# Optimization experiments

Hardware: AMD Instinct MI355X
Metric: run time of the kernel (lower is better)

The kernel has to match this reference:

```python
import jax, jax.numpy as jnp
import numpy as np

N = 100000       # nodes
E = 3200000      # edges
DIN = 128        # input_dim
H = 64           # hidden_dim
DEMB = 32        # embedding_dim
G = 256          # num graphs


def setup_inputs() -> dict:
    key = jax.random.key(0)
    ks = jax.random.split(key, 10)
    x = jax.random.normal(ks[0], (N, DIN), dtype=jnp.float32)
    edge_index = jax.random.randint(ks[1], (2, E), 0, N, dtype=jnp.int64)
    batch = jnp.sort(jax.random.randint(ks[2], (N,), 0, G, dtype=jnp.int64))
    W1 = jax.random.normal(ks[3], (DIN, H), dtype=jnp.float32) * (1.0 / np.sqrt(DIN))
    b1 = jnp.zeros((H,), dtype=jnp.float32)
    W2 = jax.random.normal(ks[4], (H, H), dtype=jnp.float32) * (1.0 / np.sqrt(H))
    b2 = jnp.zeros((H,), dtype=jnp.float32)
    Wl = jax.random.normal(ks[5], (H, DEMB), dtype=jnp.float32) * (1.0 / np.sqrt(H))
    bl = jnp.zeros((DEMB,), dtype=jnp.float32)
    return {"x": x, "edge_index": edge_index, "batch": batch, "num_graphs": G,
            "W1": W1, "b1": b1, "W2": W2, "b2": b2, "Wl": Wl, "bl": bl}


def _gcn_conv(h, src, dst, W, b, n_nodes):
    # PyG GCNConv: add self-loops, symmetric D^{-1/2}(A+I)D^{-1/2} normalization,
    # linear transform first, then propagate.
    h = h @ W                                                  # [N, out]
    deg = jax.ops.segment_sum(jnp.ones((src.shape[0],), h.dtype), dst,
                              num_segments=n_nodes) + 1.0      # +1 self-loop
    dinv = jax.lax.rsqrt(deg)                                  # [N]
    coef = dinv[src] * dinv[dst]                               # [E]
    msgs = h[src] * coef[:, None]                              # [E, out]
    agg = jax.ops.segment_sum(msgs, dst, num_segments=n_nodes)
    agg = agg + h * (dinv * dinv)[:, None]                     # self-loop message
    return agg + b


def reference(x, edge_index, batch, num_graphs, W1, b1, W2, b2, Wl, bl):
    src, dst = edge_index[0], edge_index[1]
    n_nodes = x.shape[0]
    h = jax.nn.relu(_gcn_conv(x, src, dst, W1, b1, n_nodes))
    h = jax.nn.relu(_gcn_conv(h, src, dst, W2, b2, n_nodes))
    # global_mean_pool over batch ids
    sums = jax.ops.segment_sum(h, batch, num_segments=num_graphs)     # [G, H]
    counts = jax.ops.segment_sum(jnp.ones((n_nodes,), h.dtype), batch,
                                 num_segments=num_graphs)
    pooled = sums / jnp.maximum(counts, 1.0)[:, None]
    return pooled @ Wl + bl                                           # [G, DEMB]
```

## Files before the change

### kernel.cpp

```cpp
#include <hip/hip_runtime.h>

#define NN 100000
#define NE 3200000
#define DIN 128
#define HD 64
#define DEMB 32
#define NG 256
#define NBUCK ((NN + 255) / 256)
#define NPB 512
#define CHUNK ((NE + NPB - 1) / NPB)
#define NM (NBUCK * NPB)
#define NMB ((NM + 1023) / 1024)

typedef unsigned short u16;
typedef unsigned int u32;

__device__ __forceinline__ float bflo(u32 u) { return __uint_as_float(u << 16); }
__device__ __forceinline__ float bfhi(u32 u) { return __uint_as_float(u & 0xffff0000u); }
__device__ __forceinline__ u16 f2bf(float f) {
    u32 u = __float_as_uint(f);
    return (u16)((u + 0x7fffu + ((u >> 16) & 1u)) >> 16);
}

__global__ __launch_bounds__(256) void k_blkhist(const int* __restrict__ dst,
                                                 int* __restrict__ HM, int E) {
    __shared__ int h[NBUCK];
    int blk = blockIdx.x, t = threadIdx.x;
    for (int i = t; i < NBUCK; i += 256) h[i] = 0;
    __syncthreads();
    int beg = blk * CHUNK, end = min(E, beg + CHUNK);
    for (int j = beg + t; j < end; j += 256) atomicAdd(&h[dst[j] >> 8], 1);
    __syncthreads();
    for (int i = t; i < NBUCK; i += 256) HM[i * NPB + blk] = h[i];
}

__global__ __launch_bounds__(1024) void k_scanA(int* __restrict__ HM,
                                                int* __restrict__ bsum, int n) {
    __shared__ int s[1024];
    int t = threadIdx.x;
    int idx = blockIdx.x * 1024 + t;
    int v = (idx < n) ? HM[idx] : 0;
    s[t] = v;
    __syncthreads();
    for (int off = 1; off < 1024; off <<= 1) {
        int add = (t >= off) ? s[t - off] : 0;
        __syncthreads();
        s[t] += add;
        __syncthreads();
    }
    if (idx < n) HM[idx] = s[t] - v;
    if (t == 1023) bsum[blockIdx.x] = s[t];
}

__global__ __launch_bounds__(256) void k_scan2(const int* __restrict__ bsum,
                                               int* __restrict__ boff, int nb) {
    __shared__ int s[256];
    int t = threadIdx.x;
    int v = (t < nb) ? bsum[t] : 0;
    s[t] = v;
    __syncthreads();
    for (int off = 1; off < 256; off <<= 1) {
        int add = (t >= off) ? s[t - off] : 0;
        __syncthreads();
        s[t] += add;
        __syncthreads();
    }
    if (t < nb) boff[t] = s[t] - v;
    if (t == nb - 1) boff[nb] = s[t];
}

__global__ void k_scanC(int* __restrict__ HM, const int* __restrict__ boff, int n) {
    int idx = blockIdx.x * blockDim.x + threadIdx.x;
    if (idx < n) HM[idx] += boff[idx >> 10];
}

__global__ __launch_bounds__(256) void k_place(const int* __restrict__ src,
                                               const int* __restrict__ dst,
                                               const int* __restrict__ HM,
                                               int* __restrict__ part, int E) {
    __shared__ int cur[NBUCK];
    int blk = blockIdx.x, t = threadIdx.x;
    for (int i = t; i < NBUCK; i += 256) cur[i] = HM[i * NPB + blk];
    __syncthreads();
    int beg = blk * CHUNK, end = min(E, beg + CHUNK);
    for (int j = beg + t; j < end; j += 256) {
        int d = dst[j], s = src[j];
        int pos = atomicAdd(&cur[d >> 8], 1);
        part[pos] = s | ((d & 255) << 17);
    }
}

__global__ __launch_bounds__(256) void k_phaseB(const int* __restrict__ part,
                                                const int* __restrict__ HM,
                                                int* __restrict__ rowptr,
                                                int* __restrict__ ssrc,
                                                float* __restrict__ dinv, int E) {
    __shared__ int cnt[256];
    __shared__ int sc[256];
    int b = blockIdx.x;
    int t = threadIdx.x;
    int beg = HM[b * NPB];
    int end = (b == NBUCK - 1) ? E : HM[(b + 1) * NPB];
    int node0 = b << 8;
    int nnode = NN - node0 < 256 ? NN - node0 : 256;
    cnt[t] = 0;
    __syncthreads();
    for (int j = beg + t; j < end; j += 256) atomicAdd(&cnt[part[j] >> 17], 1);
    __syncthreads();
    int v = cnt[t];
    sc[t] = v;
    __syncthreads();
    for (int off = 1; off < 256; off <<= 1) {
        int add = (t >= off) ? sc[t - off] : 0;
        __syncthreads();
        sc[t] += add;
        __syncthreads();
    }
    int excl = sc[t] - v;
    if (t < nnode) {
        rowptr[node0 + t] = beg + excl;
        dinv[node0 + t] = rsqrtf((float)v + 1.0f);
    }
    if (b == NBUCK - 1 && t == 0) rowptr[NN] = E;
    __syncthreads();
    cnt[t] = beg + excl;
    __syncthreads();
    for (int j = beg + t; j < end; j += 256) {
        int e = part[j];
        int pos = atomicAdd(&cnt[e >> 17], 1);
        ssrc[pos] = e & 0x1FFFF;
    }
}

template <int K, typename XT>
__global__ __launch_bounds__(256, 4) void k_gemm(const XT* __restrict__ X,
                                                 const float* __restrict__ W,
                                                 const float* __restrict__ dinv,
                                                 u16* __restrict__ U, int n) {
    __shared__ __align__(16) float xt[32][68];
    __shared__ __align__(16) float wlc[32][64];
    int tid = threadIdx.x;
    int cg = tid & 15;
    int rs = tid >> 4;
    int row0 = blockIdx.x * 64;
    float4 acc0 = {0.f, 0.f, 0.f, 0.f};
    float4 acc1 = {0.f, 0.f, 0.f, 0.f};
    float4 acc2 = {0.f, 0.f, 0.f, 0.f};
    float4 acc3 = {0.f, 0.f, 0.f, 0.f};
    for (int kc = 0; kc < K; kc += 32) {
        __syncthreads();
        for (int p = 0; p < 2; ++p) {
            int idx = tid + p * 256;
            int r = idx >> 3;
            int c4 = idx & 7;
            int row = row0 + r;
            float4 v = {0.f, 0.f, 0.f, 0.f};
            if (row < n) {
                if constexpr (sizeof(XT) == 4) {
                    v = *reinterpret_cast<const float4*>(&X[(size_t)row * K + kc + c4 * 4]);
                } else {
                    ushort4 b = *reinterpret_cast<const ushort4*>(&X[(size_t)row * K + kc + c4 * 4]);
                    v.x = __uint_as_float((u32)b.x << 16);
                    v.y = __uint_as_float((u32)b.y << 16);
                    v.z = __uint_as_float((u32)b.z << 16);
                    v.w = __uint_as_float((u32)b.w << 16);
                }
            }
            xt[c4 * 4 + 0][r] = v.x;
            xt[c4 * 4 + 1][r] = v.y;
            xt[c4 * 4 + 2][r] = v.z;
            xt[c4 * 4 + 3][r] = v.w;
        }
        for (int p = 0; p < 2; ++p) {
            int idx = tid + p * 256;
            int kr = idx >> 4;
            int c4 = idx & 15;
            *reinterpret_cast<float4*>(&wlc[kr][c4 * 4]) =
                *reinterpret_cast<const float4*>(&W[(size_t)(kc + kr) * 64 + c4 * 4]);
        }
        __syncthreads();
#pragma unroll
        for (int k = 0; k < 32; ++k) {
            float4 xv = *reinterpret_cast<const float4*>(&xt[k][rs * 4]);
            float4 wv = *reinterpret_cast<const float4*>(&wlc[k][cg * 4]);
            acc0.x += xv.x * wv.x; acc0.y += xv.x * wv.y; acc0.z += xv.x * wv.z; acc0.w += xv.x * wv.w;
            acc1.x += xv.y * wv.x; acc1.y += xv.y * wv.y; acc1.z += xv.y * wv.z; acc1.w += xv.y * wv.w;
            acc2.x += xv.z * wv.x; acc2.y += xv.z * wv.y; acc2.z += xv.z * wv.z; acc2.w += xv.z * wv.w;
            acc3.x += xv.w * wv.x; acc3.y += xv.w * wv.y; acc3.z += xv.w * wv.z; acc3.w += xv.w * wv.w;
        }
    }
    int rbase = row0 + rs * 4;
    float dv;
    if (rbase + 0 < n) { dv = dinv[rbase + 0];
        ushort4 o = {f2bf(acc0.x * dv), f2bf(acc0.y * dv), f2bf(acc0.z * dv), f2bf(acc0.w * dv)};
        *reinterpret_cast<ushort4*>(&U[(size_t)(rbase + 0) * 64 + cg * 4]) = o; }
    if (rbase + 1 < n) { dv = dinv[rbase + 1];
        ushort4 o = {f2bf(acc1.x * dv), f2bf(acc1.y * dv), f2bf(acc1.z * dv), f2bf(acc1.w * dv)};
        *reinterpret_cast<ushort4*>(&U[(size_t)(rbase + 1) * 64 + cg * 4]) = o; }
    if (rbase + 2 < n) { dv = dinv[rbase + 2];
        ushort4 o = {f2bf(acc2.x * dv), f2bf(acc2.y * dv), f2bf(acc2.z * dv), f2bf(acc2.w * dv)};
        *reinterpret_cast<ushort4*>(&U[(size_t)(rbase + 2) * 64 + cg * 4]) = o; }
    if (rbase + 3 < n) { dv = dinv[rbase + 3];
        ushort4 o = {f2bf(acc3.x * dv), f2bf(acc3.y * dv), f2bf(acc3.z * dv), f2bf(acc3.w * dv)};
        *reinterpret_cast<ushort4*>(&U[(size_t)(rbase + 3) * 64 + cg * 4]) = o; }
}

__global__ void k_gather(const int* __restrict__ rowptr, const int* __restrict__ ssrc,
                         const float* __restrict__ dinv, const u16* __restrict__ U,
                         const float* __restrict__ bias,
                         u16* __restrict__ outbuf, int n) {
    int gtid = blockIdx.x * blockDim.x + threadIdx.x;
    int lane = gtid & 63;
    int g = lane & 7;
    int c = lane >> 3;
    int w = gtid >> 6;
    int nw = (gridDim.x * blockDim.x) >> 6;
    float bv = bias[lane];
    for (int d = w; d < n; d += nw) {
        int beg = rowptr[d], end = rowptr[d + 1];
        float4 aL0 = {0.f,0.f,0.f,0.f}, aH0 = {0.f,0.f,0.f,0.f};
        float4 aL1 = {0.f,0.f,0.f,0.f}, aH1 = {0.f,0.f,0.f,0.f};
        int j = beg;
        for (; j + 16 <= end; j += 16) {
            int s0 = ssrc[j + g];
            int s1 = ssrc[j + 8 + g];
            uint4 u0 = *reinterpret_cast<const uint4*>(&U[(size_t)s0 * 64 + c * 8]);
            uint4 u1 = *reinterpret_cast<const uint4*>(&U[(size_t)s1 * 64 + c * 8]);
            aL0.x += bflo(u0.x); aL0.y += bfhi(u0.x); aL0.z += bflo(u0.y); aL0.w += bfhi(u0.y);
            aH0.x += bflo(u0.z); aH0.y += bfhi(u0.z); aH0.z += bflo(u0.w); aH0.w += bfhi(u0.w);
            aL1.x += bflo(u1.x); aL1.y += bfhi(u1.x); aL1.z += bflo(u1.y); aL1.w += bfhi(u1.y);
            aH1.x += bflo(u1.z); aH1.y += bfhi(u1.z); aH1.z += bflo(u1.w); aH1.w += bfhi(u1.w);
        }
        if (j + 8 <= end) {
            int s0 = ssrc[j + g];
            uint4 u0 = *reinterpret_cast<const uint4*>(&U[(size_t)s0 * 64 + c * 8]);
            aL0.x += bflo(u0.x); aL0.y += bfhi(u0.x); aL0.z += bflo(u0.y); aL0.w += bfhi(u0.y);
            aH0.x += bflo(u0.z); aH0.y += bfhi(u0.z); aH0.z += bflo(u0.w); aH0.w += bfhi(u0.w);
            j += 8;
        }
        if (j + g < end) {
            int s1 = ssrc[j + g];
            uint4 u1 = *reinterpret_cast<const uint4*>(&U[(size_t)s1 * 64 + c * 8]);
            aL1.x += bflo(u1.x); aL1.y += bfhi(u1.x); aL1.z += bflo(u1.y); aL1.w += bfhi(u1.y);
            aH1.x += bflo(u1.z); aH1.y += bfhi(u1.z); aH1.z += bflo(u1.w); aH1.w += bfhi(u1.w);
        }
        aL0.x += aL1.x; aL0.y += aL1.y; aL0.z += aL1.z; aL0.w += aL1.w;
        aH0.x += aH1.x; aH0.y += aH1.y; aH0.z += aH1.z; aH0.w += aH1.w;
#pragma unroll
        for (int m = 1; m <= 4; m <<= 1) {
            aL0.x += __shfl_xor(aL0.x, m); aL0.y += __shfl_xor(aL0.y, m);
            aL0.z += __shfl_xor(aL0.z, m); aL0.w += __shfl_xor(aL0.w, m);
            aH0.x += __shfl_xor(aH0.x, m); aH0.y += __shfl_xor(aH0.y, m);
            aH0.z += __shfl_xor(aH0.z, m); aH0.w += __shfl_xor(aH0.w, m);
        }
        float4 q = (g & 4) ? aH0 : aL0;
        float hv = (g & 2) ? ((g & 1) ? q.w : q.z) : ((g & 1) ? q.y : q.x);
        float ud = __uint_as_float(((u32)U[(size_t)d * 64 + lane]) << 16);
        float dd = dinv[d];
        float h = (hv + ud) * dd + bv;
        h = h > 0.f ? h : 0.f;
        outbuf[(size_t)d * 64 + lane] = f2bf(h);
    }
}

__global__ __launch_bounds__(256) void k_pool(const u16* __restrict__ h,
                                              const int* __restrict__ batch,
                                              float* __restrict__ sums, int n) {
    int tid = blockIdx.x * blockDim.x + threadIdx.x;
    int wave = tid >> 6;
    int lane = tid & 63;
    int node0 = wave * 64;
    if (node0 >= n) return;
    int nodeEnd = min(n, node0 + 64);
    float acc = 0.f;
    int curg = batch[node0];
    for (int nd = node0; nd < nodeEnd; ++nd) {
        int g = batch[nd];
        if (g != curg) {
            atomicAdd(&sums[(size_t)curg * 64 + lane], acc);
            acc = 0.f;
            curg = g;
        }
        acc += __uint_as_float(((u32)h[(size_t)nd * 64 + lane]) << 16);
    }
    atomicAdd(&sums[(size_t)curg * 64 + lane], acc);
}

__global__ void k_final(const float* __restrict__ sums, const int* __restrict__ batch,
                        const float* __restrict__ Wl, const float* __restrict__ bl,
                        float* __restrict__ out, int n) {
    __shared__ float pooled[64];
    int g = blockIdx.x;
    int t = threadIdx.x;
    int lo = 0, hi = n;
    while (lo < hi) { int m = (lo + hi) >> 1; if (batch[m] < g) lo = m + 1; else hi = m; }
    int lo2 = lo, hi2 = n;
    while (lo2 < hi2) { int m = (lo2 + hi2) >> 1; if (batch[m] < g + 1) lo2 = m + 1; else hi2 = m; }
    float c = (float)(lo2 - lo);
    c = c < 1.0f ? 1.0f : c;
    pooled[t] = sums[g * 64 + t] / c;
    __syncthreads();
    if (t < 32) {
        float acc = bl[t];
#pragma unroll 8
        for (int k = 0; k < 64; k++) acc += pooled[k] * Wl[k * 32 + t];
        out[g * 32 + t] = acc;
    }
}

extern "C" void kernel_launch(void* const* d_in, const int* in_sizes, int n_in,
                              void* d_out, int out_size, void* d_ws, size_t ws_size,
                              hipStream_t stream) {
    const float* x = (const float*)d_in[0];
    const int* ei = (const int*)d_in[1];
    const int* batch = (const int*)d_in[2];
    const float* W1 = (const float*)d_in[4];
    const float* b1 = (const float*)d_in[5];
    const float* W2 = (const float*)d_in[6];
    const float* b2 = (const float*)d_in[7];
    const float* Wl = (const float*)d_in[8];
    const float* bl = (const float*)d_in[9];
    float* out = (float*)d_out;

    const int* esrc = ei;
    const int* edst = ei + NE;

    char* ws = (char*)d_ws;
    size_t off = 0;
    auto alloc = [&](size_t bytes) {
        void* p = ws + off;
        off += (bytes + 255) & ~size_t(255);
        return p;
    };
    float* dinv   = (float*)alloc((size_t)NN * 4);
    int*   rowptr = (int*)alloc((size_t)(NN + 1) * 4);
    int*   HM     = (int*)alloc((size_t)NM * 4);
    int*   bsum   = (int*)alloc((size_t)(NMB + 1) * 4);
    int*   boff   = (int*)alloc((size_t)(NMB + 1) * 4);
    int*   ssrc   = (int*)alloc((size_t)NE * 4);
    u16*   tbuf   = (u16*)alloc((size_t)NE * 4);
    u16*   agg    = (u16*)alloc((size_t)NN * HD * 2);
    float* sums   = (float*)alloc((size_t)NG * HD * 4);
    int* part = (int*)tbuf;

    k_blkhist<<<NPB, 256, 0, stream>>>(edst, HM, NE);
    k_scanA<<<NMB, 1024, 0, stream>>>(HM, bsum, NM);
    k_scan2<<<1, 256, 0, stream>>>(bsum, boff, NMB);
    k_scanC<<<(NM + 255) / 256, 256, 0, stream>>>(HM, boff, NM);
    k_place<<<NPB, 256, 0, stream>>>(esrc, edst, HM, part, NE);
    k_phaseB<<<NBUCK, 256, 0, stream>>>(part, HM, rowptr, ssrc, dinv, NE);

    k_gemm<DIN, float><<<(NN + 63) / 64, 256, 0, stream>>>(x, W1, dinv, tbuf, NN);
    k_gather<<<2048, 256, 0, stream>>>(rowptr, ssrc, dinv, tbuf, b1, agg, NN);

    k_gemm<HD, u16><<<(NN + 63) / 64, 256, 0, stream>>>(agg, W2, dinv, tbuf, NN);
    k_gather<<<2048, 256, 0, stream>>>(rowptr, ssrc, dinv, tbuf, b2, agg, NN);

    hipMemsetAsync(sums, 0, (size_t)NG * HD * 4, stream);
    k_pool<<<(NN + 255) / 256, 256, 0, stream>>>(agg, batch, sums, NN);
    k_final<<<NG, 64, 0, stream>>>(sums, batch, Wl, bl, out, NN);
}
```

Measured before the change: 280.0 us.

## Use bf16 MFMA for node GEMM and deepen gather unroll to 32 edges

The feature-transform GEMM now stages X and a transposed W as bf16 in LDS and computes with 16x16x32 bf16 MFMA instructions instead of scalar FP32 FMAs. Input x is rounded to bf16 before the first layer's multiply, which adds precision loss. Separately, the edge-gather loop now processes 32 edges per iteration with four independent accumulators, to keep more gather loads in flight. The GEMM output stores become 2-byte scalar writes, which may coalesce worse than the old vector stores.

```diff
diff --git a/kernel.cpp b/kernel.cpp
--- a/kernel.cpp
+++ b/kernel.cpp
@@ -14,6 +14,8 @@
 
 typedef unsigned short u16;
 typedef unsigned int u32;
+typedef __attribute__((ext_vector_type(8))) short bf16x8;
+typedef __attribute__((ext_vector_type(4))) float f32x4;
 
 __device__ __forceinline__ float bflo(u32 u) { return __uint_as_float(u << 16); }
 __device__ __forceinline__ float bfhi(u32 u) { return __uint_as_float(u & 0xffff0000u); }
@@ -137,73 +139,64 @@
                                                  const float* __restrict__ W,
                                                  const float* __restrict__ dinv,
                                                  u16* __restrict__ U, int n) {
-    __shared__ __align__(16) float xt[32][68];
-    __shared__ __align__(16) float wlc[32][64];
+    constexpr int XS = K + 8;
+    __shared__ __align__(16) u16 xb[64 * XS];
+    __shared__ __align__(16) u16 wt[64 * XS];
     int tid = threadIdx.x;
-    int cg = tid & 15;
-    int rs = tid >> 4;
+    int lane = tid & 63, wid = tid >> 6;
     int row0 = blockIdx.x * 64;
-    float4 acc0 = {0.f, 0.f, 0.f, 0.f};
-    float4 acc1 = {0.f, 0.f, 0.f, 0.f};
-    float4 acc2 = {0.f, 0.f, 0.f, 0.f};
-    float4 acc3 = {0.f, 0.f, 0.f, 0.f};
+    for (int idx = tid; idx < 64 * (K / 4); idx += 256) {
+        int r = idx / (K / 4), c4 = idx % (K / 4);
+        int row = row0 + r;
+        ushort4 o = {0, 0, 0, 0};
+        if (row < n) {
+            if constexpr (sizeof(XT) == 4) {
+                float4 v = *reinterpret_cast<const float4*>(&X[(size_t)row * K + c4 * 4]);
+                o.x = f2bf(v.x); o.y = f2bf(v.y); o.z = f2bf(v.z); o.w = f2bf(v.w);
+            } else {
+                o = *reinterpret_cast<const ushort4*>(&X[(size_t)row * K + c4 * 4]);
+            }
+        }
+        *reinterpret_cast<ushort4*>(&xb[r * XS + c4 * 4]) = o;
+    }
+    for (int idx = tid; idx < K * 64; idx += 256) {
+        int k = idx >> 6, c = idx & 63;
+        wt[c * XS + k] = f2bf(W[(size_t)k * 64 + c]);
+    }
+    __syncthreads();
+    int lr = lane & 15, kb = lane >> 4;
+    f32x4 acc0 = {0.f, 0.f, 0.f, 0.f};
+    f32x4 acc1 = {0.f, 0.f, 0.f, 0.f};
+    f32x4 acc2 = {0.f, 0.f, 0.f, 0.f};
+    f32x4 acc3 = {0.f, 0.f, 0.f, 0.f};
+#pragma unroll
     for (int kc = 0; kc < K; kc += 32) {
-        __syncthreads();
-        for (int p = 0; p < 2; ++p) {
-            int idx = tid + p * 256;
-            int r = idx >> 3;
-            int c4 = idx & 7;
-            int row = row0 + r;
-            float4 v = {0.f, 0.f, 0.f, 0.f};
-            if (row < n) {
-                if constexpr (sizeof(XT) == 4) {
-                    v = *reinterpret_cast<const float4*>(&X[(size_t)row * K + kc + c4 * 4]);
-                } else {
-                    ushort4 b = *reinterpret_cast<const ushort4*>(&X[(size_t)row * K + kc + c4 * 4]);
-                    v.x = __uint_as_float((u32)b.x << 16);
-                    v.y = __uint_as_float((u32)b.y << 16);
-                    v.z = __uint_as_float((u32)b.z << 16);
-                    v.w = __uint_as_float((u32)b.w << 16);
-                }
-            }
-            xt[c4 * 4 + 0][r] = v.x;
-            xt[c4 * 4 + 1][r] = v.y;
-            xt[c4 * 4 + 2][r] = v.z;
-            xt[c4 * 4 + 3][r] = v.w;
-        }
-        for (int p = 0; p < 2; ++p) {
-            int idx = tid + p * 256;
-            int kr = idx >> 4;
-            int c4 = idx & 15;
-            *reinterpret_cast<float4*>(&wlc[kr][c4 * 4]) =
-                *reinterpret_cast<const float4*>(&W[(size_t)(kc + kr) * 64 + c4 * 4]);
-        }
-        __syncthreads();
+        bf16x8 a  = *reinterpret_cast<const bf16x8*>(&xb[(wid * 16 + lr) * XS + kc + kb * 8]);
+        bf16x8 b0 = *reinterpret_cast<const bf16x8*>(&wt[( 0 + lr) * XS + kc + kb * 8]);
+        bf16x8 b1 = *reinterpret_cast<const bf16x8*>(&wt[(16 + lr) * XS + kc + kb * 8]);
+        bf16x8 b2 = *reinterpret_cast<const bf16x8*>(&wt[(32 + lr) * XS + kc + kb * 8]);
+        bf16x8 b3 = *reinterpret_cast<const bf16x8*>(&wt[(48 + lr) * XS + kc + kb * 8]);
+        acc0 = __builtin_amdgcn_mfma_f32_16x16x32_bf16(a, b0, acc0, 0, 0, 0);
+        acc1 = __builtin_amdgcn_mfma_f32_16x16x32_bf16(a, b1, acc1, 0, 0, 0);
+        acc2 = __builtin_amdgcn_mfma_f32_16x16x32_bf16(a, b2, acc2, 0, 0, 0);
+        acc3 = __builtin_amdgcn_mfma_f32_16x16x32_bf16(a, b3, acc3, 0, 0, 0);
+    }
 #pragma unroll
-        for (int k = 0; k < 32; ++k) {
-            float4 xv = *reinterpret_cast<const float4*>(&xt[k][rs * 4]);
-            float4 wv = *reinterpret_cast<const float4*>(&wlc[k][cg * 4]);
-            acc0.x += xv.x * wv.x; acc0.y += xv.x * wv.y; acc0.z += xv.x * wv.z; acc0.w += xv.x * wv.w;
-            acc1.x += xv.y * wv.x; acc1.y += xv.y * wv.y; acc1.z += xv.y * wv.z; acc1.w += xv.y * wv.w;
-            acc2.x += xv.z * wv.x; acc2.y += xv.z * wv.y; acc2.z += xv.z * wv.z; acc2.w += xv.z * wv.w;
-            acc3.x += xv.w * wv.x; acc3.y += xv.w * wv.y; acc3.z += xv.w * wv.z; acc3.w += xv.w * wv.w;
-        }
-    }
-    int rbase = row0 + rs * 4;
-    float dv;
-    if (rbase + 0 < n) { dv = dinv[rbase + 0];
-        ushort4 o = {f2bf(acc0.x * dv), f2bf(acc0.y * dv), f2bf(acc0.z * dv), f2bf(acc0.w * dv)};
-        *reinterpret_cast<ushort4*>(&U[(size_t)(rbase + 0) * 64 + cg * 4]) = o; }
-    if (rbase + 1 < n) { dv = dinv[rbase + 1];
-        ushort4 o = {f2bf(acc1.x * dv), f2bf(acc1.y * dv), f2bf(acc1.z * dv), f2bf(acc1.w * dv)};
-        *reinterpret_cast<ushort4*>(&U[(size_t)(rbase + 1) * 64 + cg * 4]) = o; }
-    if (rbase + 2 < n) { dv = dinv[rbase + 2];
-        ushort4 o = {f2bf(acc2.x * dv), f2bf(acc2.y * dv), f2bf(acc2.z * dv), f2bf(acc2.w * dv)};
-        *reinterpret_cast<ushort4*>(&U[(size_t)(rbase + 2) * 64 + cg * 4]) = o; }
-    if (rbase + 3 < n) { dv = dinv[rbase + 3];
-        ushort4 o = {f2bf(acc3.x * dv), f2bf(acc3.y * dv), f2bf(acc3.z * dv), f2bf(acc3.w * dv)};
-        *reinterpret_cast<ushort4*>(&U[(size_t)(rbase + 3) * 64 + cg * 4]) = o; }
-}
+    for (int reg = 0; reg < 4; ++reg) {
+        int row = row0 + wid * 16 + kb * 4 + reg;
+        if (row < n) {
+            float dv = dinv[row];
+            U[(size_t)row * 64 +  0 + lr] = f2bf(acc0[reg] * dv);
+            U[(size_t)row * 64 + 16 + lr] = f2bf(acc1[reg] * dv);
+            U[(size_t)row * 64 + 32 + lr] = f2bf(acc2[reg] * dv);
+            U[(size_t)row * 64 + 48 + lr] = f2bf(acc3[reg] * dv);
+        }
+    }
+}
+
+#define ACC8(u, L, H) \
+    L.x += bflo(u.x); L.y += bfhi(u.x); L.z += bflo(u.y); L.w += bfhi(u.y); \
+    H.x += bflo(u.z); H.y += bfhi(u.z); H.z += bflo(u.w); H.w += bfhi(u.w);
 
 __global__ void k_gather(const int* __restrict__ rowptr, const int* __restrict__ ssrc,
                          const float* __restrict__ dinv, const u16* __restrict__ U,
@@ -220,40 +213,57 @@
         int beg = rowptr[d], end = rowptr[d + 1];
         float4 aL0 = {0.f,0.f,0.f,0.f}, aH0 = {0.f,0.f,0.f,0.f};
         float4 aL1 = {0.f,0.f,0.f,0.f}, aH1 = {0.f,0.f,0.f,0.f};
+        float4 aL2 = {0.f,0.f,0.f,0.f}, aH2 = {0.f,0.f,0.f,0.f};
+        float4 aL3 = {0.f,0.f,0.f,0.f}, aH3 = {0.f,0.f,0.f,0.f};
         int j = beg;
-        for (; j + 16 <= end; j += 16) {
+        for (; j + 32 <= end; j += 32) {
+            int s0 = ssrc[j + g];
+            int s1 = ssrc[j + 8 + g];
+            int s2 = ssrc[j + 16 + g];
+            int s3 = ssrc[j + 24 + g];
+            uint4 u0 = *reinterpret_cast<const uint4*>(&U[(size_t)s0 * 64 + c * 8]);
+            uint4 u1 = *reinterpret_cast<const uint4*>(&U[(size_t)s1 * 64 + c * 8]);
+            uint4 u2 = *reinterpret_cast<const uint4*>(&U[(size_t)s2 * 64 + c * 8]);
+            uint4 u3 = *reinterpret_cast<const uint4*>(&U[(size_t)s3 * 64 + c * 8]);
+            ACC8(u0, aL0, aH0); ACC8(u1, aL1, aH1);
+            ACC8(u2, aL2, aH2); ACC8(u3, aL3, aH3);
+        }
+        if (j + 16 <= end) {
             int s0 = ssrc[j + g];
             int s1 = ssrc[j + 8 + g];
             uint4 u0 = *reinterpret_cast<const uint4*>(&U[(size_t)s0 * 64 + c * 8]);
             uint4 u1 = *reinterpret_cast<const uint4*>(&U[(size_t)s1 * 64 + c * 8]);
-            aL0.x += bflo(u0.x); aL0.y += bfhi(u0.x); aL0.z += bflo(u0.y); aL0.w += bfhi(u0.y);
-            aH0.x += bflo(u0.z); aH0.y += bfhi(u0.z); aH0.z += bflo(u0.w); aH0.w += bfhi(u0.w);
-            aL1.x += bflo(u1.x); aL1.y += bfhi(u1.x); aL1.z += bflo(u1.y); aL1.w += bfhi(u1.y);
-            aH1.x += bflo(u1.z); aH1.y += bfhi(u1.z); aH1.z += bflo(u1.w); aH1.w += bfhi(u1.w);
+            ACC8(u0, aL0, aH0); ACC8(u1, aL1, aH1);
+            j += 16;
         }
         if (j + 8 <= end) {
-            int s0 = ssrc[j + g];
-            uint4 u0 = *reinterpret_cast<const uint4*>(&U[(size_t)s0 * 64 + c * 8]);
-            aL0.x += bflo(u0.x); aL0.y += bfhi(u0.x); aL0.z += bflo(u0.y); aL0.w += bfhi(u0.y);
-            aH0.x += bflo(u0.z); aH0.y += bfhi(u0.z); aH0.z += bflo(u0.w); aH0.w += bfhi(u0.w);
+            int s2 = ssrc[j + g];
+            uint4 u2 = *reinterpret_cast<const uint4*>(&U[(size_t)s2 * 64 + c * 8]);
+            ACC8(u2, aL2, aH2);
             j += 8;
         }
         if (j + g < end) {
-            int s1 = ssrc[j + g];
-            uint4 u1 = *reinterpret_cast<const uint4*>(&U[(size_t)s1 * 64 + c * 8]);
-            aL1.x += bflo(u1.x); aL1.y += bfhi(u1.x); aL1.z += bflo(u1.y); aL1.w += bfhi(u1.y);
-            aH1.x += bflo(u1.z); aH1.y += bfhi(u1.z); aH1.z += bflo(u1.w); aH1.w += bfhi(u1.w);
-        }
-        aL0.x += aL1.x; aL0.y += aL1.y; aL0.z += aL1.z; aL0.w += aL1.w;
-        aH0.x += aH1.x; aH0.y += aH1.y; aH0.z += aH1.z; aH0.w += aH1.w;
+            int s3 = ssrc[j + g];
+            uint4 u3 = *reinterpret_cast<const uint4*>(&U[(size_t)s3 * 64 + c * 8]);
+            ACC8(u3, aL3, aH3);
+        }
+        float4 aL, aH;
+        aL.x = (aL0.x + aL1.x) + (aL2.x + aL3.x);
+        aL.y = (aL0.y + aL1.y) + (aL2.y + aL3.y);
+        aL.z = (aL0.z + aL1.z) + (aL2.z + aL3.z);
+        aL.w = (aL0.w + aL1.w) + (aL2.w + aL3.w);
+        aH.x = (aH0.x + aH1.x) + (aH2.x + aH3.x);
+        aH.y = (aH0.y + aH1.y) + (aH2.y + aH3.y);
+        aH.z = (aH0.z + aH1.z) + (aH2.z + aH3.z);
+        aH.w = (aH0.w + aH1.w) + (aH2.w + aH3.w);
 #pragma unroll
         for (int m = 1; m <= 4; m <<= 1) {
-            aL0.x += __shfl_xor(aL0.x, m); aL0.y += __shfl_xor(aL0.y, m);
-            aL0.z += __shfl_xor(aL0.z, m); aL0.w += __shfl_xor(aL0.w, m);
-            aH0.x += __shfl_xor(aH0.x, m); aH0.y += __shfl_xor(aH0.y, m);
-            aH0.z += __shfl_xor(aH0.z, m); aH0.w += __shfl_xor(aH0.w, m);
-        }
-        float4 q = (g & 4) ? aH0 : aL0;
+            aL.x += __shfl_xor(aL.x, m); aL.y += __shfl_xor(aL.y, m);
+            aL.z += __shfl_xor(aL.z, m); aL.w += __shfl_xor(aL.w, m);
+            aH.x += __shfl_xor(aH.x, m); aH.y += __shfl_xor(aH.y, m);
+            aH.z += __shfl_xor(aH.z, m); aH.w += __shfl_xor(aH.w, m);
+        }
+        float4 q = (g & 4) ? aH : aL;
         float hv = (g & 2) ? ((g & 1) ? q.w : q.z) : ((g & 1) ? q.y : q.x);
         float ud = __uint_as_float(((u32)U[(size_t)d * 64 + lane]) << 16);
         float dd = dinv[d];
```

Result: slower. 314.3 us (+12.2%).
